# Performance work log

Measured on AMD Instinct MI355X. Metric: run time of the kernel, lower is better.

## Reference

```python
import jax, jax.numpy as jnp
import numpy as np


def setup_inputs() -> dict:
    key = jax.random.key(0)
    ks = jax.random.split(key, 18)
    V, E, H, T = 32000, 512, 1024, 256
    s_e = 1.0 / np.sqrt(E)
    s_h = 1.0 / np.sqrt(H)
    inp = {
        "encoding": jax.random.normal(ks[0], (1, H), jnp.float32),
        "tokens": jax.random.randint(ks[1], (T,), 0, V),
        "embedding": jax.random.normal(ks[2], (V, E), jnp.float32),
        "wzx_w": jax.random.normal(ks[3], (H, E), jnp.float32) * s_e,
        "wzx_b": jax.random.normal(ks[4], (H,), jnp.float32) * s_e,
        "wrx_w": jax.random.normal(ks[5], (H, E), jnp.float32) * s_e,
        "wrx_b": jax.random.normal(ks[6], (H,), jnp.float32) * s_e,
        "whx_w": jax.random.normal(ks[7], (H, E), jnp.float32) * s_e,
        "whx_b": jax.random.normal(ks[8], (H,), jnp.float32) * s_e,
        "wzh_w": jax.random.normal(ks[9], (H, H), jnp.float32) * s_h,
        "wzh_b": jax.random.normal(ks[10], (H,), jnp.float32) * s_h,
        "wrh_w": jax.random.normal(ks[11], (H, H), jnp.float32) * s_h,
        "wrh_b": jax.random.normal(ks[12], (H,), jnp.float32) * s_h,
        "whh_w": jax.random.normal(ks[13], (H, H), jnp.float32) * s_h,
        "whh_b": jax.random.normal(ks[14], (H,), jnp.float32) * s_h,
        "out_w": jax.random.normal(ks[15], (V, H), jnp.float32) * s_h,
        "out_b": jax.random.normal(ks[16], (V,), jnp.float32) * s_h,
    }
    return inp


def reference(encoding, tokens, embedding,
              wzx_w, wzx_b, wrx_w, wrx_b, whx_w, whx_b,
              wzh_w, wzh_b, wrh_w, wrh_b, whh_w, whh_b,
              out_w, out_b):
    # Teacher-forced GRU decode: tokens[t] is the 'previous word' fed at step t.
    def step(h, tok):
        e = embedding[tok][None, :]                                   # [1, E]
        z = jax.nn.sigmoid(e @ wzx_w.T + wzx_b + h @ wzh_w.T + wzh_b)  # [1, H]
        r = jax.nn.sigmoid(e @ wrx_w.T + wrx_b + h @ wrh_w.T + wrh_b)
        h_prime = jnp.tanh(e @ whx_w.T + whx_b + (r * h) @ whh_w.T + whh_b)
        h_new = (1.0 - z) * h + z * h_prime
        logits = h_new @ out_w.T + out_b                               # [1, V]
        return h_new, logits

    _, output_vectors = jax.lax.scan(step, encoding, tokens)          # [T, 1, V]
    pred_ids = jnp.argmax(output_vectors, axis=-1)                    # [T, 1]
    return output_vectors, pred_ids
```

## Files before the change

### kernel.cpp

```cpp
#include <hip/hip_runtime.h>
#include <hip/hip_bf16.h>
#include <math.h>

constexpr int T_STEPS = 256;
constexpr int HDIM    = 1024;
constexpr int EDIM    = 512;
constexpr int VDIM    = 32000;

#define RG     128
#define RROWS  8

constexpr size_t WS_BZ     = 0;
constexpr size_t WS_BR     = WS_BZ + (size_t)T_STEPS * HDIM;
constexpr size_t WS_A      = WS_BR + (size_t)T_STEPS * HDIM;
constexpr size_t WS_HPACK  = WS_A  + (size_t)T_STEPS * HDIM;
constexpr size_t WS_RHPACK = WS_HPACK + (size_t)2 * (T_STEPS + 1) * HDIM;
constexpr size_t WS_HSEQ   = WS_BZ;

__device__ __forceinline__ float sigmoidf_(float x) { return 1.0f / (1.0f + __expf(-x)); }

__device__ __forceinline__ unsigned long long pack_tv(int tag, float v) {
  return ((unsigned long long)(unsigned)tag << 32) | (unsigned long long)__float_as_uint(v);
}

__global__ __launch_bounds__(256) void k_init(const float* __restrict__ enc, float* __restrict__ ws) {
  unsigned long long* hpack  = (unsigned long long*)(ws + WS_HPACK);
  unsigned long long* rhpack = (unsigned long long*)(ws + WS_RHPACK);
  const int b = blockIdx.x, tid = threadIdx.x;
  if (b == 0) {
    for (int i = tid; i < HDIM; i += 256) hpack[i] = pack_tv(1, enc[i]);
  } else if (b <= T_STEPS) {
    unsigned long long* row = hpack + (size_t)b * HDIM;
    for (int i = tid; i < HDIM; i += 256) row[i] = 0ULL;
  } else {
    for (int i = tid; i < HDIM; i += 256) rhpack[i] = 0ULL;
  }
}

__global__ __launch_bounds__(256) void k_xproj(
    const int* __restrict__ tokens, const float* __restrict__ emb,
    const float* __restrict__ wzx, const float* __restrict__ wrx, const float* __restrict__ whx,
    const float* __restrict__ bzx, const float* __restrict__ bzh,
    const float* __restrict__ brx, const float* __restrict__ brh,
    const float* __restrict__ bhx, const float* __restrict__ bhh,
    float* __restrict__ ws) {
  __shared__ __align__(16) float es[16][EDIM];
  const int b   = blockIdx.x;
  const int t0  = (b & 15) * 16;
  const int c   = b >> 4;
  const int tid = threadIdx.x;

  {
    int row = tid >> 4;
    int kc  = (tid & 15) * 32;
    int tok = tokens[t0 + row];
    const float4* ep = (const float4*)(emb + (size_t)tok * EDIM + kc);
    float4* dst = (float4*)&es[row][kc];
    #pragma unroll
    for (int q = 0; q < 8; q++) dst[q] = ep[q];
  }
  __syncthreads();

  const int mat = c >> 2;
  const int j   = (c & 3) * 256 + tid;
  const float* W; const float* b1; const float* b2; float* Xout;
  if (mat == 0)      { W = wzx; b1 = bzx; b2 = bzh; Xout = ws + WS_BZ; }
  else if (mat == 1) { W = wrx; b1 = brx; b2 = brh; Xout = ws + WS_BR; }
  else               { W = whx; b1 = bhx; b2 = bhh; Xout = ws + WS_A;  }

  const float4* wp = (const float4*)(W + (size_t)j * EDIM);
  const float bias = b1[j] + b2[j];
  float acc[16];
  #pragma unroll
  for (int tt = 0; tt < 16; tt++) acc[tt] = 0.0f;

  for (int k4 = 0; k4 < EDIM / 4; k4++) {
    float4 w = wp[k4];
    #pragma unroll
    for (int tt = 0; tt < 16; tt++) {
      float4 e4 = *(const float4*)&es[tt][k4 * 4];
      acc[tt] += w.x * e4.x + w.y * e4.y + w.z * e4.z + w.w * e4.w;
    }
  }
  #pragma unroll
  for (int tt = 0; tt < 16; tt++)
    Xout[(size_t)(t0 + tt) * HDIM + j] = acc[tt] + bias;
}

__global__ __launch_bounds__(256) void k_recur(
    const float* __restrict__ wzh, const float* __restrict__ wrh, const float* __restrict__ whh,
    float* __restrict__ ws) {
  const int g    = blockIdx.x;
  const int tid  = threadIdx.x;
  const int lane = tid & 63;
  const int wv   = tid >> 6;
  const float* Bz = ws + WS_BZ;
  const float* Br = ws + WS_BR;
  const float* Aa = ws + WS_A;
  float* hseq = ws + WS_HSEQ;
  unsigned long long* hpack  = (unsigned long long*)(ws + WS_HPACK);
  unsigned long long* rhpack = (unsigned long long*)(ws + WS_RHPACK);

  const int j0 = 4 * tid;
  const int r0 = g * RROWS;

  float4 wz[RROWS], wr[RROWS], wh[RROWS];
  #pragma unroll
  for (int k = 0; k < RROWS; k++) {
    wz[k] = *(const float4*)(wzh + (size_t)(r0 + k) * HDIM + j0);
    wr[k] = *(const float4*)(wrh + (size_t)(r0 + k) * HDIM + j0);
    wh[k] = *(const float4*)(whh + (size_t)(r0 + k) * HDIM + j0);
  }

  __shared__ float red[4][2 * RROWS];
  __shared__ float zs[RROWS];
  __shared__ float hloc[RROWS];
  if (tid < RROWS)
    hloc[tid] = __uint_as_float((unsigned)hpack[r0 + tid]);
  __syncthreads();

  for (int t = 0; t < T_STEPS; t++) {
    float bz_pre = 0.0f, br_pre = 0.0f, a_pre = 0.0f;
    if (tid < RROWS) {
      bz_pre = Bz[(size_t)t * HDIM + r0 + tid];
      a_pre  = Aa[(size_t)t * HDIM + r0 + tid];
    } else if (tid < 2 * RROWS) {
      br_pre = Br[(size_t)t * HDIM + r0 + (tid - RROWS)];
    }
    const unsigned long long ex = (unsigned long long)(unsigned)(t + 1);

    float hv0, hv1, hv2, hv3;
    {
      const unsigned long long* hp = hpack + (size_t)t * HDIM + j0;
      unsigned long long w0, w1, w2, w3;
      int it = 0;
      for (;;) {
        w0 = __hip_atomic_load(hp + 0, __ATOMIC_RELAXED, __HIP_MEMORY_SCOPE_AGENT);
        w1 = __hip_atomic_load(hp + 1, __ATOMIC_RELAXED, __HIP_MEMORY_SCOPE_AGENT);
        w2 = __hip_atomic_load(hp + 2, __ATOMIC_RELAXED, __HIP_MEMORY_SCOPE_AGENT);
        w3 = __hip_atomic_load(hp + 3, __ATOMIC_RELAXED, __HIP_MEMORY_SCOPE_AGENT);
        if (((w0 >> 32) == ex) & ((w1 >> 32) == ex) & ((w2 >> 32) == ex) & ((w3 >> 32) == ex)) break;
        if (++it > (1 << 20)) break;
        __builtin_amdgcn_s_sleep(1);
      }
      hv0 = __uint_as_float((unsigned)w0);
      hv1 = __uint_as_float((unsigned)w1);
      hv2 = __uint_as_float((unsigned)w2);
      hv3 = __uint_as_float((unsigned)w3);
    }

    float pz[RROWS], pr[RROWS];
    #pragma unroll
    for (int k = 0; k < RROWS; k++) {
      pz[k] = wz[k].x * hv0 + wz[k].y * hv1 + wz[k].z * hv2 + wz[k].w * hv3;
      pr[k] = wr[k].x * hv0 + wr[k].y * hv1 + wr[k].z * hv2 + wr[k].w * hv3;
    }
    #pragma unroll
    for (int m = 32; m >= 1; m >>= 1) {
      #pragma unroll
      for (int k = 0; k < RROWS; k++) {
        pz[k] += __shfl_xor(pz[k], m);
        pr[k] += __shfl_xor(pr[k], m);
      }
    }
    if (lane == 0) {
      #pragma unroll
      for (int k = 0; k < RROWS; k++) { red[wv][k] = pz[k]; red[wv][RROWS + k] = pr[k]; }
    }
    __syncthreads();
    if (tid < RROWS) {
      float u = red[0][tid] + red[1][tid] + red[2][tid] + red[3][tid];
      zs[tid] = sigmoidf_(bz_pre + u);
    } else if (tid < 2 * RROWS) {
      int k = tid - RROWS;
      float u = red[0][tid] + red[1][tid] + red[2][tid] + red[3][tid];
      float r = sigmoidf_(br_pre + u);
      float rh = r * hloc[k];
      __hip_atomic_store(&rhpack[r0 + k], pack_tv(t + 1, rh),
                         __ATOMIC_RELAXED, __HIP_MEMORY_SCOPE_AGENT);
    }

    float rv0, rv1, rv2, rv3;
    {
      const unsigned long long* rp = rhpack + j0;
      unsigned long long w0, w1, w2, w3;
      int it = 0;
      for (;;) {
        w0 = __hip_atomic_load(rp + 0, __ATOMIC_RELAXED, __HIP_MEMORY_SCOPE_AGENT);
        w1 = __hip_atomic_load(rp + 1, __ATOMIC_RELAXED, __HIP_MEMORY_SCOPE_AGENT);
        w2 = __hip_atomic_load(rp + 2, __ATOMIC_RELAXED, __HIP_MEMORY_SCOPE_AGENT);
        w3 = __hip_atomic_load(rp + 3, __ATOMIC_RELAXED, __HIP_MEMORY_SCOPE_AGENT);
        if (((w0 >> 32) == ex) & ((w1 >> 32) == ex) & ((w2 >> 32) == ex) & ((w3 >> 32) == ex)) break;
        if (++it > (1 << 20)) break;
        __builtin_amdgcn_s_sleep(1);
      }
      rv0 = __uint_as_float((unsigned)w0);
      rv1 = __uint_as_float((unsigned)w1);
      rv2 = __uint_as_float((unsigned)w2);
      rv3 = __uint_as_float((unsigned)w3);
    }

    float ph[RROWS];
    #pragma unroll
    for (int k = 0; k < RROWS; k++)
      ph[k] = wh[k].x * rv0 + wh[k].y * rv1 + wh[k].z * rv2 + wh[k].w * rv3;
    #pragma unroll
    for (int m = 32; m >= 1; m >>= 1) {
      #pragma unroll
      for (int k = 0; k < RROWS; k++) ph[k] += __shfl_xor(ph[k], m);
    }
    if (lane == 0) {
      #pragma unroll
      for (int k = 0; k < RROWS; k++) red[wv][k] = ph[k];
    }
    __syncthreads();
    if (tid < RROWS) {
      float v  = red[0][tid] + red[1][tid] + red[2][tid] + red[3][tid];
      float z  = zs[tid];
      float hk = hloc[tid];
      float hp_ = tanhf(a_pre + v);
      float hn = (1.0f - z) * hk + z * hp_;
      hloc[tid] = hn;
      __hip_atomic_store(&hpack[(size_t)(t + 1) * HDIM + r0 + tid], pack_tv(t + 2, hn),
                         __ATOMIC_RELAXED, __HIP_MEMORY_SCOPE_AGENT);
      hseq[(size_t)t * HDIM + r0 + tid] = hn;
    }
  }
}

__global__ __launch_bounds__(256) void k_gemm(
    const float* __restrict__ hseq, const float* __restrict__ outw,
    const float* __restrict__ outb, float* __restrict__ out) {
  __shared__ __align__(16) float As[16][132];
  __shared__ __align__(16) float Bs[16][132];
  const int tid = threadIdx.x;
  const int m0 = blockIdx.x * 128;
  const int n0 = blockIdx.y * 128;
  const int tx = tid & 15, ty = tid >> 4;
  const int lr = tid >> 1;
  const int lc = (tid & 1) * 8;
  const float* Ag = hseq + (size_t)(m0 + lr) * HDIM + lc;
  const float* Bg = outw + (size_t)(n0 + lr) * HDIM + lc;

  float acc[8][8];
  #pragma unroll
  for (int i = 0; i < 8; i++)
    #pragma unroll
    for (int j = 0; j < 8; j++) acc[i][j] = 0.0f;

  for (int k0 = 0; k0 < HDIM; k0 += 16) {
    float4 a0 = *(const float4*)(Ag + k0);
    float4 a1 = *(const float4*)(Ag + k0 + 4);
    float4 b0 = *(const float4*)(Bg + k0);
    float4 b1 = *(const float4*)(Bg + k0 + 4);
    __syncthreads();
    As[lc + 0][lr] = a0.x; As[lc + 1][lr] = a0.y; As[lc + 2][lr] = a0.z; As[lc + 3][lr] = a0.w;
    As[lc + 4][lr] = a1.x; As[lc + 5][lr] = a1.y; As[lc + 6][lr] = a1.z; As[lc + 7][lr] = a1.w;
    Bs[lc + 0][lr] = b0.x; Bs[lc + 1][lr] = b0.y; Bs[lc + 2][lr] = b0.z; Bs[lc + 3][lr] = b0.w;
    Bs[lc + 4][lr] = b1.x; Bs[lc + 5][lr] = b1.y; Bs[lc + 6][lr] = b1.z; Bs[lc + 7][lr] = b1.w;
    __syncthreads();
    #pragma unroll
    for (int kk = 0; kk < 16; kk++) {
      float4 av0 = *(const float4*)&As[kk][ty * 8];
      float4 av1 = *(const float4*)&As[kk][ty * 8 + 4];
      float4 bv0 = *(const float4*)&Bs[kk][tx * 8];
      float4 bv1 = *(const float4*)&Bs[kk][tx * 8 + 4];
      float am[8] = {av0.x, av0.y, av0.z, av0.w, av1.x, av1.y, av1.z, av1.w};
      float bn[8] = {bv0.x, bv0.y, bv0.z, bv0.w, bv1.x, bv1.y, bv1.z, bv1.w};
      #pragma unroll
      for (int i = 0; i < 8; i++)
        #pragma unroll
        for (int j = 0; j < 8; j++) acc[i][j] += am[i] * bn[j];
    }
  }

  float4 ob0 = *(const float4*)(outb + n0 + tx * 8);
  float4 ob1 = *(const float4*)(outb + n0 + tx * 8 + 4);
  float bn[8] = {ob0.x, ob0.y, ob0.z, ob0.w, ob1.x, ob1.y, ob1.z, ob1.w};
  #pragma unroll
  for (int i = 0; i < 8; i++) {
    int row = m0 + ty * 8 + i;
    float* op = out + (size_t)row * VDIM + n0 + tx * 8;
    float4 c0 = make_float4(acc[i][0] + bn[0], acc[i][1] + bn[1], acc[i][2] + bn[2], acc[i][3] + bn[3]);
    float4 c1 = make_float4(acc[i][4] + bn[4], acc[i][5] + bn[5], acc[i][6] + bn[6], acc[i][7] + bn[7]);
    *(float4*)op = c0;
    *(float4*)(op + 4) = c1;
  }
}

__global__ __launch_bounds__(256) void k_argmax(const float* __restrict__ logits,
                                                float* __restrict__ outids) {
  const int t = blockIdx.x;
  const int tid = threadIdx.x;
  const float* row = logits + (size_t)t * VDIM;
  float best = -3.4e38f; int bi = 0;
  for (int v = tid; v < VDIM; v += 256) {
    float x = row[v];
    if (x > best) { best = x; bi = v; }
  }
  __shared__ float bv[256];
  __shared__ int  bidx[256];
  bv[tid] = best; bidx[tid] = bi;
  __syncthreads();
  for (int s = 128; s > 0; s >>= 1) {
    if (tid < s) {
      if (bv[tid + s] > bv[tid] || (bv[tid + s] == bv[tid] && bidx[tid + s] < bidx[tid])) {
        bv[tid] = bv[tid + s]; bidx[tid] = bidx[tid + s];
      }
    }
    __syncthreads();
  }
  if (tid == 0) outids[t] = (float)bidx[0];
}

extern "C" void kernel_launch(void* const* d_in, const int* in_sizes, int n_in,
                              void* d_out, int out_size, void* d_ws, size_t ws_size,
                              hipStream_t stream) {
  (void)in_sizes; (void)n_in; (void)out_size; (void)ws_size;
  const float* enc    = (const float*)d_in[0];
  const int*   tokens = (const int*)d_in[1];
  const float* emb    = (const float*)d_in[2];
  const float* wzx_w  = (const float*)d_in[3];
  const float* wzx_b  = (const float*)d_in[4];
  const float* wrx_w  = (const float*)d_in[5];
  const float* wrx_b  = (const float*)d_in[6];
  const float* whx_w  = (const float*)d_in[7];
  const float* whx_b  = (const float*)d_in[8];
  const float* wzh_w  = (const float*)d_in[9];
  const float* wzh_b  = (const float*)d_in[10];
  const float* wrh_w  = (const float*)d_in[11];
  const float* wrh_b  = (const float*)d_in[12];
  const float* whh_w  = (const float*)d_in[13];
  const float* whh_b  = (const float*)d_in[14];
  const float* out_w  = (const float*)d_in[15];
  const float* out_b  = (const float*)d_in[16];
  float* ws  = (float*)d_ws;
  float* out = (float*)d_out;

  k_init<<<dim3(T_STEPS + 2), dim3(256), 0, stream>>>(enc, ws);
  k_xproj<<<dim3(192), dim3(256), 0, stream>>>(tokens, emb, wzx_w, wrx_w, whx_w,
                                               wzx_b, wzh_b, wrx_b, wrh_b, whx_b, whh_b, ws);
  k_recur<<<dim3(RG), dim3(256), 0, stream>>>(wzh_w, wrh_w, whh_w, ws);
  k_gemm<<<dim3(2, 250), dim3(256), 0, stream>>>(ws + WS_HSEQ, out_w, out_b, out);
  k_argmax<<<dim3(256), dim3(256), 0, stream>>>(out, out + (size_t)T_STEPS * VDIM);
}
```

Before: 1.498 ms.

## Use bf16 MFMA for output projection with fp32 argmax candidate re-check

```diff
diff --git a/kernel.cpp b/kernel.cpp
--- a/kernel.cpp
+++ b/kernel.cpp
@@ -16,11 +16,20 @@
 constexpr size_t WS_HPACK  = WS_A  + (size_t)T_STEPS * HDIM;
 constexpr size_t WS_RHPACK = WS_HPACK + (size_t)2 * (T_STEPS + 1) * HDIM;
 constexpr size_t WS_HSEQ   = WS_BZ;
+constexpr size_t WS_HSEQB  = WS_BR;
+
+typedef __attribute__((ext_vector_type(8))) short short8;
+typedef __attribute__((ext_vector_type(4))) float f32x4;
 
 __device__ __forceinline__ float sigmoidf_(float x) { return 1.0f / (1.0f + __expf(-x)); }
 
 __device__ __forceinline__ unsigned long long pack_tv(int tag, float v) {
   return ((unsigned long long)(unsigned)tag << 32) | (unsigned long long)__float_as_uint(v);
+}
+
+__device__ __forceinline__ unsigned short f2bf(float f) {
+  unsigned u = __float_as_uint(f);
+  return (unsigned short)((u + 0x7FFFu + ((u >> 16) & 1u)) >> 16);
 }
 
 __global__ __launch_bounds__(256) void k_init(const float* __restrict__ enc, float* __restrict__ ws) {
@@ -98,6 +107,7 @@
   const float* Br = ws + WS_BR;
   const float* Aa = ws + WS_A;
   float* hseq = ws + WS_HSEQ;
+  unsigned short* hseqb = (unsigned short*)(ws + WS_HSEQB);
   unsigned long long* hpack  = (unsigned long long*)(ws + WS_HPACK);
   unsigned long long* rhpack = (unsigned long long*)(ws + WS_RHPACK);
 
@@ -112,7 +122,8 @@
     wh[k] = *(const float4*)(whh + (size_t)(r0 + k) * HDIM + j0);
   }
 
-  __shared__ float red[4][2 * RROWS];
+  __shared__ float redA[4][2 * RROWS];
+  __shared__ float redB[4][RROWS];
   __shared__ float zs[RROWS];
   __shared__ float hloc[RROWS];
   if (tid < RROWS)
@@ -136,10 +147,15 @@
       int it = 0;
       for (;;) {
         w0 = __hip_atomic_load(hp + 0, __ATOMIC_RELAXED, __HIP_MEMORY_SCOPE_AGENT);
+        if ((w0 >> 32) == ex) break;
+        if (++it > (1 << 20)) break;
+        __builtin_amdgcn_s_sleep(2);
+      }
+      for (;;) {
         w1 = __hip_atomic_load(hp + 1, __ATOMIC_RELAXED, __HIP_MEMORY_SCOPE_AGENT);
         w2 = __hip_atomic_load(hp + 2, __ATOMIC_RELAXED, __HIP_MEMORY_SCOPE_AGENT);
         w3 = __hip_atomic_load(hp + 3, __ATOMIC_RELAXED, __HIP_MEMORY_SCOPE_AGENT);
-        if (((w0 >> 32) == ex) & ((w1 >> 32) == ex) & ((w2 >> 32) == ex) & ((w3 >> 32) == ex)) break;
+        if (((w1 >> 32) == ex) & ((w2 >> 32) == ex) & ((w3 >> 32) == ex)) break;
         if (++it > (1 << 20)) break;
         __builtin_amdgcn_s_sleep(1);
       }
@@ -165,15 +181,15 @@
     }
     if (lane == 0) {
       #pragma unroll
-      for (int k = 0; k < RROWS; k++) { red[wv][k] = pz[k]; red[wv][RROWS + k] = pr[k]; }
+      for (int k = 0; k < RROWS; k++) { redA[wv][k] = pz[k]; redA[wv][RROWS + k] = pr[k]; }
     }
     __syncthreads();
     if (tid < RROWS) {
-      float u = red[0][tid] + red[1][tid] + red[2][tid] + red[3][tid];
+      float u = redA[0][tid] + redA[1][tid] + redA[2][tid] + redA[3][tid];
       zs[tid] = sigmoidf_(bz_pre + u);
     } else if (tid < 2 * RROWS) {
       int k = tid - RROWS;
-      float u = red[0][tid] + red[1][tid] + red[2][tid] + red[3][tid];
+      float u = redA[0][tid] + redA[1][tid] + redA[2][tid] + redA[3][tid];
       float r = sigmoidf_(br_pre + u);
       float rh = r * hloc[k];
       __hip_atomic_store(&rhpack[r0 + k], pack_tv(t + 1, rh),
@@ -187,10 +203,15 @@
       int it = 0;
       for (;;) {
         w0 = __hip_atomic_load(rp + 0, __ATOMIC_RELAXED, __HIP_MEMORY_SCOPE_AGENT);
+        if ((w0 >> 32) == ex) break;
+        if (++it > (1 << 20)) break;
+        __builtin_amdgcn_s_sleep(2);
+      }
+      for (;;) {
         w1 = __hip_atomic_load(rp + 1, __ATOMIC_RELAXED, __HIP_MEMORY_SCOPE_AGENT);
         w2 = __hip_atomic_load(rp + 2, __ATOMIC_RELAXED, __HIP_MEMORY_SCOPE_AGENT);
         w3 = __hip_atomic_load(rp + 3, __ATOMIC_RELAXED, __HIP_MEMORY_SCOPE_AGENT);
-        if (((w0 >> 32) == ex) & ((w1 >> 32) == ex) & ((w2 >> 32) == ex) & ((w3 >> 32) == ex)) break;
+        if (((w1 >> 32) == ex) & ((w2 >> 32) == ex) & ((w3 >> 32) == ex)) break;
         if (++it > (1 << 20)) break;
         __builtin_amdgcn_s_sleep(1);
       }
@@ -211,11 +232,11 @@
     }
     if (lane == 0) {
       #pragma unroll
-      for (int k = 0; k < RROWS; k++) red[wv][k] = ph[k];
+      for (int k = 0; k < RROWS; k++) redB[wv][k] = ph[k];
     }
     __syncthreads();
     if (tid < RROWS) {
-      float v  = red[0][tid] + red[1][tid] + red[2][tid] + red[3][tid];
+      float v  = redB[0][tid] + redB[1][tid] + redB[2][tid] + redB[3][tid];
       float z  = zs[tid];
       float hk = hloc[tid];
       float hp_ = tanhf(a_pre + v);
@@ -224,93 +245,130 @@
       __hip_atomic_store(&hpack[(size_t)(t + 1) * HDIM + r0 + tid], pack_tv(t + 2, hn),
                          __ATOMIC_RELAXED, __HIP_MEMORY_SCOPE_AGENT);
       hseq[(size_t)t * HDIM + r0 + tid] = hn;
+      hseqb[(size_t)t * HDIM + r0 + tid] = f2bf(hn);
     }
   }
 }
 
 __global__ __launch_bounds__(256) void k_gemm(
-    const float* __restrict__ hseq, const float* __restrict__ outw,
+    const unsigned short* __restrict__ Abf, const float* __restrict__ outw,
     const float* __restrict__ outb, float* __restrict__ out) {
-  __shared__ __align__(16) float As[16][132];
-  __shared__ __align__(16) float Bs[16][132];
-  const int tid = threadIdx.x;
-  const int m0 = blockIdx.x * 128;
-  const int n0 = blockIdx.y * 128;
-  const int tx = tid & 15, ty = tid >> 4;
-  const int lr = tid >> 1;
-  const int lc = (tid & 1) * 8;
-  const float* Ag = hseq + (size_t)(m0 + lr) * HDIM + lc;
-  const float* Bg = outw + (size_t)(n0 + lr) * HDIM + lc;
-
-  float acc[8][8];
-  #pragma unroll
-  for (int i = 0; i < 8; i++)
-    #pragma unroll
-    for (int j = 0; j < 8; j++) acc[i][j] = 0.0f;
-
-  for (int k0 = 0; k0 < HDIM; k0 += 16) {
-    float4 a0 = *(const float4*)(Ag + k0);
-    float4 a1 = *(const float4*)(Ag + k0 + 4);
-    float4 b0 = *(const float4*)(Bg + k0);
-    float4 b1 = *(const float4*)(Bg + k0 + 4);
-    __syncthreads();
-    As[lc + 0][lr] = a0.x; As[lc + 1][lr] = a0.y; As[lc + 2][lr] = a0.z; As[lc + 3][lr] = a0.w;
-    As[lc + 4][lr] = a1.x; As[lc + 5][lr] = a1.y; As[lc + 6][lr] = a1.z; As[lc + 7][lr] = a1.w;
-    Bs[lc + 0][lr] = b0.x; Bs[lc + 1][lr] = b0.y; Bs[lc + 2][lr] = b0.z; Bs[lc + 3][lr] = b0.w;
-    Bs[lc + 4][lr] = b1.x; Bs[lc + 5][lr] = b1.y; Bs[lc + 6][lr] = b1.z; Bs[lc + 7][lr] = b1.w;
-    __syncthreads();
-    #pragma unroll
-    for (int kk = 0; kk < 16; kk++) {
-      float4 av0 = *(const float4*)&As[kk][ty * 8];
-      float4 av1 = *(const float4*)&As[kk][ty * 8 + 4];
-      float4 bv0 = *(const float4*)&Bs[kk][tx * 8];
-      float4 bv1 = *(const float4*)&Bs[kk][tx * 8 + 4];
-      float am[8] = {av0.x, av0.y, av0.z, av0.w, av1.x, av1.y, av1.z, av1.w};
-      float bn[8] = {bv0.x, bv0.y, bv0.z, bv0.w, bv1.x, bv1.y, bv1.z, bv1.w};
-      #pragma unroll
-      for (int i = 0; i < 8; i++)
-        #pragma unroll
-        for (int j = 0; j < 8; j++) acc[i][j] += am[i] * bn[j];
-    }
-  }
-
-  float4 ob0 = *(const float4*)(outb + n0 + tx * 8);
-  float4 ob1 = *(const float4*)(outb + n0 + tx * 8 + 4);
-  float bn[8] = {ob0.x, ob0.y, ob0.z, ob0.w, ob1.x, ob1.y, ob1.z, ob1.w};
-  #pragma unroll
-  for (int i = 0; i < 8; i++) {
-    int row = m0 + ty * 8 + i;
-    float* op = out + (size_t)row * VDIM + n0 + tx * 8;
-    float4 c0 = make_float4(acc[i][0] + bn[0], acc[i][1] + bn[1], acc[i][2] + bn[2], acc[i][3] + bn[3]);
-    float4 c1 = make_float4(acc[i][4] + bn[4], acc[i][5] + bn[5], acc[i][6] + bn[6], acc[i][7] + bn[7]);
-    *(float4*)op = c0;
-    *(float4*)(op + 4) = c1;
+  const int tid  = threadIdx.x;
+  const int lane = tid & 63;
+  const int wv   = tid >> 6;
+  const int n0   = blockIdx.x * 128;
+  const int rA   = lane & 15;
+  const int kg   = lane >> 4;
+
+  f32x4 acc[4][8];
+  #pragma unroll
+  for (int i = 0; i < 4; i++)
+    #pragma unroll
+    for (int j = 0; j < 8; j++) acc[i][j] = (f32x4){0.f, 0.f, 0.f, 0.f};
+
+  const int mbase = wv * 64 + rA;
+
+  for (int k0 = 0; k0 < HDIM; k0 += 32) {
+    const int ks = k0 + kg * 8;
+    short8 afr[4];
+    #pragma unroll
+    for (int i = 0; i < 4; i++)
+      afr[i] = *(const short8*)(Abf + (size_t)(mbase + i * 16) * HDIM + ks);
+
+    short8 bfr[8];
+    #pragma unroll
+    for (int j = 0; j < 8; j++) {
+      const float* bp = outw + (size_t)(n0 + j * 16 + rA) * HDIM + ks;
+      float4 b0 = *(const float4*)(bp);
+      float4 b1 = *(const float4*)(bp + 4);
+      short8 s;
+      s[0] = (short)f2bf(b0.x); s[1] = (short)f2bf(b0.y);
+      s[2] = (short)f2bf(b0.z); s[3] = (short)f2bf(b0.w);
+      s[4] = (short)f2bf(b1.x); s[5] = (short)f2bf(b1.y);
+      s[6] = (short)f2bf(b1.z); s[7] = (short)f2bf(b1.w);
+      bfr[j] = s;
+    }
+
+    #pragma unroll
+    for (int i = 0; i < 4; i++)
+      #pragma unroll
+      for (int j = 0; j < 8; j++)
+        acc[i][j] = __builtin_amdgcn_mfma_f32_16x16x32_bf16(afr[i], bfr[j], acc[i][j], 0, 0, 0);
+  }
+
+  float bias[8];
+  #pragma unroll
+  for (int j = 0; j < 8; j++) bias[j] = outb[n0 + j * 16 + rA];
+  #pragma unroll
+  for (int i = 0; i < 4; i++) {
+    #pragma unroll
+    for (int j = 0; j < 8; j++) {
+      #pragma unroll
+      for (int r = 0; r < 4; r++) {
+        int m = wv * 64 + i * 16 + kg * 4 + r;
+        out[(size_t)m * VDIM + n0 + j * 16 + rA] = acc[i][j][r] + bias[j];
+      }
+    }
   }
 }
 
 __global__ __launch_bounds__(256) void k_argmax(const float* __restrict__ logits,
+                                                const float* __restrict__ hseqf,
+                                                const float* __restrict__ outw,
+                                                const float* __restrict__ outb,
                                                 float* __restrict__ outids) {
   const int t = blockIdx.x;
   const int tid = threadIdx.x;
   const float* row = logits + (size_t)t * VDIM;
-  float best = -3.4e38f; int bi = 0;
+
+  float mx = -3.4e38f;
+  for (int v = tid; v < VDIM; v += 256) mx = fmaxf(mx, row[v]);
+  __shared__ float sm[256];
+  sm[tid] = mx;
+  __syncthreads();
+  for (int s = 128; s > 0; s >>= 1) {
+    if (tid < s) sm[tid] = fmaxf(sm[tid], sm[tid + s]);
+    __syncthreads();
+  }
+  const float bmax = sm[0];
+  __syncthreads();
+
+  __shared__ int cand[64];
+  __shared__ int cnt;
+  if (tid == 0) cnt = 0;
+  __syncthreads();
+  const float cut = bmax - 0.25f;
   for (int v = tid; v < VDIM; v += 256) {
-    float x = row[v];
-    if (x > best) { best = x; bi = v; }
-  }
-  __shared__ float bv[256];
-  __shared__ int  bidx[256];
-  bv[tid] = best; bidx[tid] = bi;
-  __syncthreads();
-  for (int s = 128; s > 0; s >>= 1) {
-    if (tid < s) {
-      if (bv[tid + s] > bv[tid] || (bv[tid + s] == bv[tid] && bidx[tid + s] < bidx[tid])) {
-        bv[tid] = bv[tid + s]; bidx[tid] = bidx[tid + s];
-      }
-    }
-    __syncthreads();
-  }
-  if (tid == 0) outids[t] = (float)bidx[0];
+    if (row[v] >= cut) {
+      int p = atomicAdd(&cnt, 1);
+      if (p < 64) cand[p] = v;
+    }
+  }
+  __syncthreads();
+  int n = cnt < 64 ? cnt : 64;
+
+  __shared__ float cval[64];
+  if (tid < n) {
+    int v = cand[tid];
+    const float* w = outw + (size_t)v * HDIM;
+    const float* h = hseqf + (size_t)t * HDIM;
+    float s0 = 0.f, s1 = 0.f, s2 = 0.f, s3 = 0.f;
+    for (int k = 0; k < HDIM; k += 4) {
+      float4 wf = *(const float4*)(w + k);
+      float4 hf = *(const float4*)(h + k);
+      s0 += wf.x * hf.x; s1 += wf.y * hf.y; s2 += wf.z * hf.z; s3 += wf.w * hf.w;
+    }
+    cval[tid] = (s0 + s1) + (s2 + s3) + outb[v];
+  }
+  __syncthreads();
+  if (tid == 0) {
+    float best = -3.4e38f; int bi = 0x7FFFFFFF;
+    for (int i = 0; i < n; i++) {
+      float v = cval[i]; int id = cand[i];
+      if (v > best || (v == best && id < bi)) { best = v; bi = id; }
+    }
+    outids[t] = (float)bi;
+  }
 }
 
 extern "C" void kernel_launch(void* const* d_in, const int* in_sizes, int n_in,
@@ -341,6 +399,8 @@
   k_xproj<<<dim3(192), dim3(256), 0, stream>>>(tokens, emb, wzx_w, wrx_w, whx_w,
                                                wzx_b, wzh_b, wrx_b, wrh_b, whx_b, whh_b, ws);
   k_recur<<<dim3(RG), dim3(256), 0, stream>>>(wzh_w, wrh_w, whh_w, ws);
-  k_gemm<<<dim3(2, 250), dim3(256), 0, stream>>>(ws + WS_HSEQ, out_w, out_b, out);
-  k_argmax<<<dim3(256), dim3(256), 0, stream>>>(out, out + (size_t)T_STEPS * VDIM);
-}
+  k_gemm<<<dim3(VDIM / 128), dim3(256), 0, stream>>>((const unsigned short*)(ws + WS_HSEQB),
+                                                     out_w, out_b, out);
+  k_argmax<<<dim3(T_STEPS), dim3(256), 0, stream>>>(out, ws + WS_HSEQ, out_w, out_b,
+                                                    out + (size_t)T_STEPS * VDIM);
+}
```

Result: faster. 1.435 ms (-4.2%).
